# Performance work log

Hardware: AMD Instinct MI355X
Metric: run time of the kernel (lower is better)

The kernel has to match this reference:

```python
import jax, jax.numpy as jnp
import numpy as np

B, L, D = 16, 1024, 1024
OUT_LEN = 24
N_LAYERS = 3
CYCLE = L
LN_EPS = 1e-5


def _make_pe(seq_len, hidden, cycle):
    # pe[t, j] = 2*pi*t/cycle, then sin on even cols, cos on odd cols
    t = jnp.arange(seq_len, dtype=jnp.float32)[:, None]
    base = (2.0 * jnp.pi * t / cycle) * jnp.ones((1, hidden), jnp.float32)
    cols = jnp.arange(hidden)
    return jnp.where((cols % 2 == 0)[None, :], jnp.sin(base), jnp.cos(base))


def setup_inputs() -> dict:
    key = jax.random.key(0)
    ks = jax.random.split(key, 12)
    s = 0.02
    return {
        "x": jax.random.normal(ks[0], (B, L, D), jnp.float32),
        "pe": _make_pe(L, D, CYCLE),
        "w1": jax.random.normal(ks[1], (N_LAYERS, D, D), jnp.float32) * s,
        "b1": jnp.zeros((N_LAYERS, D), jnp.float32),
        "w2": jax.random.normal(ks[2], (N_LAYERS, D, D), jnp.float32) * s,
        "b2": jnp.zeros((N_LAYERS, D), jnp.float32),
        "ln_g": jnp.ones((N_LAYERS, D), jnp.float32),
        "ln_b": jnp.zeros((N_LAYERS, D), jnp.float32),
        "fc_w": jax.random.normal(ks[3], (1, D), jnp.float32) * s,
        "fc_b": jnp.zeros((1,), jnp.float32),
        "final_w": jax.random.normal(ks[4], (OUT_LEN, L), jnp.float32) * s,
        "final_b": jnp.zeros((OUT_LEN,), jnp.float32),
    }


def _layer_norm(y, g, b):
    mu = jnp.mean(y, axis=-1, keepdims=True)
    var = jnp.mean((y - mu) ** 2, axis=-1, keepdims=True)
    return (y - mu) * jax.lax.rsqrt(var + LN_EPS) * g + b


def reference(x, pe, w1, b1, w2, b2, ln_g, ln_b, fc_w, fc_b, final_w, final_b):
    d = x.shape[-1]
    scale = 1.0 / jnp.sqrt(jnp.float32(d))
    # positional add (pe[:, :seq_len]; here L == D so this is the full buffer)
    h = x + pe[:, : x.shape[1]]
    attns = []
    for l in range(w1.shape[0]):
        # hand-rolled bmm-softmax-bmm self-attention (q = k = v = h)
        scores = jnp.einsum("bqd,bkd->bqk", h, h) * scale  # (B, L, L)
        a = jax.nn.softmax(scores, axis=-1)
        ctx = jnp.einsum("bqk,bkd->bqd", a, h)
        # position-wise FFN with hidden == D, residual over ctx, then LN
        ff = jnp.maximum(ctx @ w1[l].T + b1[l], 0.0) @ w2[l].T + b2[l]
        h = _layer_norm(ctx + ff, ln_g[l], ln_b[l])
        attns.append(a)
    # final head: D -> 1, squeeze, then L -> OUT_LEN over the sequence dim
    z = (h @ fc_w.T + fc_b)[..., 0]  # (B, L)
    out = z @ final_w.T + final_b    # (B, OUT_LEN)
    return (out, jnp.stack(attns))
```

## Files before the change

### kernel.cpp

```cpp
#include <hip/hip_runtime.h>

typedef unsigned short u16;
typedef __attribute__((ext_vector_type(8))) short short8;
typedef __attribute__((ext_vector_type(4))) float f32x4;
typedef __attribute__((ext_vector_type(4))) unsigned short u16x4;

__device__ __forceinline__ float bf2f(u16 u){
  union { unsigned int i; float f; } x; x.i = ((unsigned int)u) << 16; return x.f;
}
__device__ __forceinline__ u16 f2bf(float f){
  union { float f; unsigned int i; } x; x.f = f;
  return (u16)((x.i + 0x7fffu + ((x.i >> 16) & 1u)) >> 16);
}
__device__ __forceinline__ void async16(const void* g, void* s){
  __builtin_amdgcn_global_load_lds((const __attribute__((address_space(1))) void*)g,
                                   (__attribute__((address_space(3))) void*)s, 16, 0, 0);
}

__global__ __launch_bounds__(256) void k_split(const float* __restrict__ s, u16* __restrict__ d){
  long i = ((long)blockIdx.x * 256 + threadIdx.x) * 4;
  f32x4 v = *(const f32x4*)(s + i);
  u16x4 hh;
  #pragma unroll
  for (int j=0;j<4;j++) hh[j] = f2bf(v[j]);
  *(u16x4*)(d+i) = hh;
}

__global__ __launch_bounds__(256) void k_addpe(const float* __restrict__ x, const float* __restrict__ pe,
                                               u16* __restrict__ d){
  long i = ((long)blockIdx.x * 256 + threadIdx.x) * 4;
  f32x4 xv = *(const f32x4*)(x + i);
  f32x4 pv = *(const f32x4*)(pe + (i & 1048575));
  u16x4 hh;
  #pragma unroll
  for (int j=0;j<4;j++) hh[j] = f2bf(xv[j]+pv[j]);
  *(u16x4*)(d+i) = hh;
}

__global__ __launch_bounds__(256) void k_transpose(const u16* __restrict__ in, u16* __restrict__ outp){
  __shared__ u16 tile[64][68];
  const long b = blockIdx.z;
  const int d0 = blockIdx.x * 64, l0 = blockIdx.y * 64;
  const long ibase = b * 1048576l;
  const int t = threadIdx.x;
  const int cr = t >> 4;
  const int cc = (t & 15) * 4;
  #pragma unroll
  for (int rr=0; rr<4; rr++){
    int row = cr + rr*16;
    u16x4 v = *(const u16x4*)(in + ibase + (long)(l0+row)*1024 + d0 + cc);
    *(u16x4*)&tile[row][cc] = v;
  }
  __syncthreads();
  #pragma unroll
  for (int rr=0; rr<4; rr++){
    int drow = cr + rr*16;
    u16x4 y;
    y[0] = tile[cc+0][drow];
    y[1] = tile[cc+1][drow];
    y[2] = tile[cc+2][drow];
    y[3] = tile[cc+3][drow];
    *(u16x4*)(outp + ibase + (long)(d0+drow)*1024 + l0 + cc) = y;
  }
}

template<int MODE>
__global__ __launch_bounds__(256) void gemm1(
    const u16* __restrict__ aB, const u16* __restrict__ bB,
    int K, int lda, int ldb, int ldc,
    long strideA, long strideB, long strideC,
    int gridN, int gridM,
    float scale, const float* __restrict__ bias,
    const u16* __restrict__ res,
    float* __restrict__ cF, u16* __restrict__ cB)
{
  __shared__ __align__(16) u16 sm[8192];
  const int t = threadIdx.x;
  const int w = t >> 6;
  const int lane = t & 63;

  const int p = blockIdx.x;
  const int chunk = gridDim.x >> 3;
  const int id = (p & 7) * chunk + (p >> 3);
  const int per = gridN * gridM;
  const long bz = id / per;
  const int rem = id % per;
  const int m0 = (rem / gridN) << 7, n0 = (rem % gridN) << 7;

  const u16* a = aB + bz * strideA;
  const u16* b = bB + bz * strideB;

  const int rA0 = t >> 2;
  const int rA1 = 64 + rA0;
  const int s0 = (t & 3) ^ ((rA0 >> 1) & 3);
  const int s1 = (t & 3) ^ ((rA1 >> 1) & 3);
  const u16* gA0 = a + (long)(m0 + rA0) * lda + s0 * 8;
  const u16* gA1 = a + (long)(m0 + rA1) * lda + s1 * 8;
  const u16* gB0 = b + (long)(n0 + rA0) * ldb + s0 * 8;
  const u16* gB1 = b + (long)(n0 + rA1) * ldb + s1 * 8;
  u16* ldsW = sm + (w << 9);

  f32x4 acc[4][4];
  #pragma unroll
  for (int i=0;i<4;i++)
    #pragma unroll
    for (int j=0;j<4;j++) acc[i][j] = (f32x4){0.f,0.f,0.f,0.f};

  const int fr = lane & 15, fs = lane >> 4;
  int offA[4], offB[4];
  #pragma unroll
  for (int i=0;i<4;i++){
    int ra = (w >> 1)*64 + i*16 + fr;
    offA[i] = ra*32 + (fs ^ ((ra>>1)&3))*8;
    int rb = (w & 1)*64 + i*16 + fr;
    offB[i] = rb*32 + (fs ^ ((rb>>1)&3))*8;
  }

  for (int k0 = 0; k0 < K; k0 += 32){
    async16(gA0 + k0, ldsW + 0);
    async16(gA1 + k0, ldsW + 2048);
    async16(gB0 + k0, ldsW + 4096);
    async16(gB1 + k0, ldsW + 6144);
    __syncthreads();
    short8 ah[4];
    #pragma unroll
    for (int i=0;i<4;i++) ah[i] = *(const short8*)(sm + offA[i]);
    #pragma unroll
    for (int j=0;j<4;j++){
      short8 bh = *(const short8*)(sm + 4096 + offB[j]);
      #pragma unroll
      for (int i=0;i<4;i++)
        acc[i][j] = __builtin_amdgcn_mfma_f32_16x16x32_bf16(ah[i], bh, acc[i][j], 0,0,0);
    }
    __syncthreads();
  }

  const long cBase = bz * strideC;
  const int colb = n0 + (w & 1)*64 + fr;
  const int rowb = m0 + (w >> 1)*64 + fs*4;
  #pragma unroll
  for (int j=0;j<4;j++){
    const int c = colb + j*16;
    float bv = 0.f;
    if constexpr (MODE == 2 || MODE == 3) bv = bias[c];
    #pragma unroll
    for (int i=0;i<4;i++){
      #pragma unroll
      for (int q=0;q<4;q++){
        const int r = rowb + i*16 + q;
        const long idx = cBase + (long)r*ldc + c;
        float v = acc[i][j][q];
        if constexpr (MODE == 0){
          cF[idx] = v * scale;
        } else if constexpr (MODE == 1){
          cB[idx] = f2bf(v);
        } else if constexpr (MODE == 2){
          cB[idx] = f2bf(fmaxf(v + bv, 0.f));
        } else {
          cF[idx] = v + bv + bf2f(res[idx]);
        }
      }
    }
  }
}

__global__ __launch_bounds__(256) void k_softmax(float* __restrict__ p, u16* __restrict__ pB){
  const long row = blockIdx.x;
  float* pr = p + row * 1024;
  const int t = threadIdx.x, w = t >> 6, lane = t & 63;
  __shared__ float rA[4], rB[4];
  f32x4 v = *(const f32x4*)(pr + t*4);
  float m = fmaxf(fmaxf(v[0],v[1]), fmaxf(v[2],v[3]));
  #pragma unroll
  for (int off=32; off; off>>=1) m = fmaxf(m, __shfl_xor(m, off));
  if (lane==0) rA[w] = m;
  __syncthreads();
  m = fmaxf(fmaxf(rA[0],rA[1]), fmaxf(rA[2],rA[3]));
  float e[4]; float s = 0.f;
  #pragma unroll
  for (int j=0;j<4;j++){ e[j] = expf(v[j]-m); s += e[j]; }
  #pragma unroll
  for (int off=32; off; off>>=1) s += __shfl_xor(s, off);
  if (lane==0) rB[w] = s;
  __syncthreads();
  s = rB[0]+rB[1]+rB[2]+rB[3];
  const float inv = 1.0f / s;
  f32x4 o; u16x4 hh;
  #pragma unroll
  for (int j=0;j<4;j++){
    float pv = e[j]*inv; o[j] = pv; hh[j] = f2bf(pv);
  }
  *(f32x4*)(pr + t*4) = o;
  *(u16x4*)(pB + row*1024 + t*4) = hh;
}

__global__ __launch_bounds__(256) void k_ln(const float* __restrict__ r,
                                            const float* __restrict__ g, const float* __restrict__ b,
                                            u16* __restrict__ h){
  const long row = blockIdx.x;
  const float* rr = r + row * 1024;
  const int t = threadIdx.x, w = t >> 6, lane = t & 63;
  __shared__ float rA[4], rB[4];
  f32x4 v = *(const f32x4*)(rr + t*4);
  float s = v[0]+v[1]+v[2]+v[3];
  #pragma unroll
  for (int off=32; off; off>>=1) s += __shfl_xor(s, off);
  if (lane==0) rA[w] = s;
  __syncthreads();
  const float mu = (rA[0]+rA[1]+rA[2]+rA[3]) * (1.0f/1024.0f);
  float sq = 0.f;
  #pragma unroll
  for (int j=0;j<4;j++){ float d = v[j]-mu; sq += d*d; }
  #pragma unroll
  for (int off=32; off; off>>=1) sq += __shfl_xor(sq, off);
  if (lane==0) rB[w] = sq;
  __syncthreads();
  const float var = (rB[0]+rB[1]+rB[2]+rB[3]) * (1.0f/1024.0f);
  const float inv = rsqrtf(var + 1e-5f);
  u16x4 hh;
  #pragma unroll
  for (int j=0;j<4;j++){
    int d = t*4+j;
    hh[j] = f2bf((v[j]-mu)*inv*g[d] + b[d]);
  }
  *(u16x4*)(h + row*1024 + t*4) = hh;
}

__global__ __launch_bounds__(256) void k_final1(const u16* __restrict__ h,
                                                const float* __restrict__ fw, const float* __restrict__ fb,
                                                float* __restrict__ z){
  const int row = blockIdx.x*4 + (threadIdx.x>>6);
  const int lane = threadIdx.x & 63;
  const long base = (long)row * 1024;
  const int d0 = lane * 16;
  float s = 0.f;
  #pragma unroll
  for (int j=0;j<16;j++){
    int d = d0 + j;
    s += bf2f(h[base+d]) * fw[d];
  }
  #pragma unroll
  for (int off=32; off; off>>=1) s += __shfl_xor(s, off);
  if (lane==0) z[row] = s + fb[0];
}

__global__ __launch_bounds__(256) void k_final2(const float* __restrict__ z,
                                                const float* __restrict__ fw, const float* __restrict__ fb,
                                                float* __restrict__ out){
  const int idx = blockIdx.x*4 + (threadIdx.x>>6);
  const int lane = threadIdx.x & 63;
  const int b = idx / 24, o = idx % 24;
  float s = 0.f;
  #pragma unroll
  for (int j=0;j<16;j++){
    int li = lane + j*64;
    s += z[b*1024 + li] * fw[o*1024 + li];
  }
  #pragma unroll
  for (int off=32; off; off>>=1) s += __shfl_xor(s, off);
  if (lane==0) out[idx] = s + fb[o];
}

extern "C" void kernel_launch(void* const* d_in, const int* in_sizes, int n_in,
                              void* d_out, int out_size, void* d_ws, size_t ws_size,
                              hipStream_t stream){
  const float* x   = (const float*)d_in[0];
  const float* pe  = (const float*)d_in[1];
  const float* w1  = (const float*)d_in[2];
  const float* b1  = (const float*)d_in[3];
  const float* w2  = (const float*)d_in[4];
  const float* b2  = (const float*)d_in[5];
  const float* lng = (const float*)d_in[6];
  const float* lnb = (const float*)d_in[7];
  const float* fcw = (const float*)d_in[8];
  const float* fcb = (const float*)d_in[9];
  const float* fw  = (const float*)d_in[10];
  const float* fb  = (const float*)d_in[11];
  float* out  = (float*)d_out;
  float* attn = out + 384;

  char* ws = (char*)d_ws;
  const long BB = 32l*1024*1024;
  u16* hB = (u16*)(ws + 0*BB);
  u16* tB = (u16*)(ws + 1*BB);
  u16* cB = (u16*)(ws + 2*BB);
  u16* pB = (u16*)(ws + 3*BB);
  float* rf = (float*)(ws + 4*BB);
  u16* w1B = (u16*)(ws + 6*BB);
  u16* w2B = w1B + 3l*1024*1024;
  float* z = (float*)(w2B + 3l*1024*1024);

  const long M1 = 1024l*1024;

  k_split<<<3072, 256, 0, stream>>>(w1, w1B);
  k_split<<<3072, 256, 0, stream>>>(w2, w2B);
  k_addpe<<<16384, 256, 0, stream>>>(x, pe, hB);
  k_transpose<<<dim3(16,16,16), 256, 0, stream>>>(hB, tB);

  for (int l = 0; l < 3; l++){
    float* sc = attn + (long)l*16*M1;
    gemm1<0><<<1024, 256, 0, stream>>>(hB, hB, 1024,1024,1024,1024,
        M1,M1,M1, 8,8, 0.03125f, nullptr, nullptr, sc, nullptr);
    k_softmax<<<16384, 256, 0, stream>>>(sc, pB);
    gemm1<1><<<1024, 256, 0, stream>>>(pB, tB, 1024,1024,1024,1024,
        M1,M1,M1, 8,8, 1.f, nullptr, nullptr, nullptr, cB);
    gemm1<2><<<1024, 256, 0, stream>>>(cB, w1B+l*M1, 1024,1024,1024,1024,
        0,0,0, 8,128, 1.f, b1+l*1024, nullptr, nullptr, pB);
    gemm1<3><<<1024, 256, 0, stream>>>(pB, w2B+l*M1, 1024,1024,1024,1024,
        0,0,0, 8,128, 1.f, b2+l*1024, cB, rf, nullptr);
    k_ln<<<16384, 256, 0, stream>>>(rf, lng+l*1024, lnb+l*1024, hB);
    if (l < 2) k_transpose<<<dim3(16,16,16), 256, 0, stream>>>(hB, tB);
  }

  k_final1<<<4096, 256, 0, stream>>>(hB, fcw, fcb, z);
  k_final2<<<96, 256, 0, stream>>>(z, fw, fb, out);
}
```

Baseline: 881.6 us.

## Replace 128x128 GEMM with 256x256 tile, 4-stage async LDS pipeline

Replaces the 256-thread 128x128-tile GEMM, which synchronized on every K step, with a 512-thread, 8-wave kernel computing 256x256 tiles. It keeps a 4-deep ring of LDS buffers filled by async global-to-LDS loads, uses explicit vmcnt waits and barriers, and raises wave priority around the MFMA bursts. The aim is to hide global load latency and raise data reuse per tile. In exchange it uses 128 KB of LDS and 128 accumulator floats per thread. It also hardcodes K=1024 (32 K-steps), so the grid drops to 256 blocks, which may underfill the 256 CUs.

```diff
diff --git a/kernel.cpp b/kernel.cpp
--- a/kernel.cpp
+++ b/kernel.cpp
@@ -65,89 +65,156 @@
 }
 
 template<int MODE>
-__global__ __launch_bounds__(256) void gemm1(
+__global__ __launch_bounds__(512, 2) void gemm8(
     const u16* __restrict__ aB, const u16* __restrict__ bB,
-    int K, int lda, int ldb, int ldc,
-    long strideA, long strideB, long strideC,
-    int gridN, int gridM,
+    int per, long sA, long sB, long sC,
+    int lda, int ldb, int ldc,
     float scale, const float* __restrict__ bias,
     const u16* __restrict__ res,
     float* __restrict__ cF, u16* __restrict__ cB)
 {
-  __shared__ __align__(16) u16 sm[8192];
+  __shared__ __align__(16) u16 sm[65536];
   const int t = threadIdx.x;
-  const int w = t >> 6;
-  const int lane = t & 63;
+  const int w = t >> 6, lane = t & 63;
+  const int wm = w >> 2, wn = w & 3;
+  const int fr = lane & 15, fs = lane >> 4;
 
   const int p = blockIdx.x;
   const int chunk = gridDim.x >> 3;
   const int id = (p & 7) * chunk + (p >> 3);
-  const int per = gridN * gridM;
   const long bz = id / per;
   const int rem = id % per;
-  const int m0 = (rem / gridN) << 7, n0 = (rem % gridN) << 7;
-
-  const u16* a = aB + bz * strideA;
-  const u16* b = bB + bz * strideB;
-
-  const int rA0 = t >> 2;
-  const int rA1 = 64 + rA0;
-  const int s0 = (t & 3) ^ ((rA0 >> 1) & 3);
-  const int s1 = (t & 3) ^ ((rA1 >> 1) & 3);
-  const u16* gA0 = a + (long)(m0 + rA0) * lda + s0 * 8;
-  const u16* gA1 = a + (long)(m0 + rA1) * lda + s1 * 8;
-  const u16* gB0 = b + (long)(n0 + rA0) * ldb + s0 * 8;
-  const u16* gB1 = b + (long)(n0 + rA1) * ldb + s1 * 8;
-  u16* ldsW = sm + (w << 9);
-
-  f32x4 acc[4][4];
-  #pragma unroll
-  for (int i=0;i<4;i++)
+  const int m0 = (rem >> 2) << 8, n0 = (rem & 3) << 8;
+
+  const u16* a = aB + bz * sA;
+  const u16* b = bB + bz * sB;
+
+  const int urow = t >> 2;
+  const int col8 = ((t & 3) ^ ((t >> 3) & 3)) * 8;
+  const u16* gA0 = a + (long)(m0 + urow) * lda + col8;
+  const u16* gA1 = a + (long)(m0 + 128 + urow) * lda + col8;
+  const u16* gB0 = b + (long)(n0 + urow) * ldb + col8;
+  const u16* gB1 = b + (long)(n0 + 128 + urow) * ldb + col8;
+  u16* dA0 = sm + (w << 9);
+  u16* dA1 = sm + 4096 + (w << 9);
+  u16* dB0 = sm + 8192 + (w << 9);
+  u16* dB1 = sm + 12288 + (w << 9);
+
+  int offA[8], offB[4];
+  #pragma unroll
+  for (int i=0;i<8;i++){
+    int row = wm*128 + i*16 + fr;
+    int sl = fs ^ ((row >> 1) & 3);
+    offA[i] = row*32 + sl*8;
+  }
+  #pragma unroll
+  for (int j=0;j<4;j++){
+    int row = wn*64 + j*16 + fr;
+    int sl = fs ^ ((row >> 1) & 3);
+    offB[j] = 8192 + row*32 + sl*8;
+  }
+
+  f32x4 acc[8][4];
+  #pragma unroll
+  for (int i=0;i<8;i++)
     #pragma unroll
     for (int j=0;j<4;j++) acc[i][j] = (f32x4){0.f,0.f,0.f,0.f};
 
-  const int fr = lane & 15, fs = lane >> 4;
-  int offA[4], offB[4];
-  #pragma unroll
-  for (int i=0;i<4;i++){
-    int ra = (w >> 1)*64 + i*16 + fr;
-    offA[i] = ra*32 + (fs ^ ((ra>>1)&3))*8;
-    int rb = (w & 1)*64 + i*16 + fr;
-    offB[i] = rb*32 + (fs ^ ((rb>>1)&3))*8;
-  }
-
-  for (int k0 = 0; k0 < K; k0 += 32){
-    async16(gA0 + k0, ldsW + 0);
-    async16(gA1 + k0, ldsW + 2048);
-    async16(gB0 + k0, ldsW + 4096);
-    async16(gB1 + k0, ldsW + 6144);
-    __syncthreads();
-    short8 ah[4];
-    #pragma unroll
-    for (int i=0;i<4;i++) ah[i] = *(const short8*)(sm + offA[i]);
-    #pragma unroll
-    for (int j=0;j<4;j++){
-      short8 bh = *(const short8*)(sm + 4096 + offB[j]);
-      #pragma unroll
-      for (int i=0;i<4;i++)
-        acc[i][j] = __builtin_amdgcn_mfma_f32_16x16x32_bf16(ah[i], bh, acc[i][j], 0,0,0);
-    }
-    __syncthreads();
-  }
-
-  const long cBase = bz * strideC;
-  const int colb = n0 + (w & 1)*64 + fr;
-  const int rowb = m0 + (w >> 1)*64 + fs*4;
+  #pragma unroll
+  for (int pb=0; pb<3; ++pb){
+    const int kb = pb*32, sb = pb*16384;
+    async16(gA0+kb, dA0+sb); async16(gA1+kb, dA1+sb);
+    async16(gB0+kb, dB0+sb); async16(gB1+kb, dB1+sb);
+  }
+  gA0 += 96; gA1 += 96; gB0 += 96; gB1 += 96;
+  asm volatile("s_waitcnt vmcnt(8)" ::: "memory");
+  __builtin_amdgcn_s_barrier();
+  __builtin_amdgcn_sched_barrier(0);
+
+#define KT_COMPUTE(SMB)                                                        \
+    short8 aF[8];                                                              \
+    _Pragma("unroll")                                                          \
+    for (int i=0;i<8;i++) aF[i] = *(const short8*)((SMB) + offA[i]);           \
+    short8 bF0 = *(const short8*)((SMB) + offB[0]);                            \
+    short8 bF1 = *(const short8*)((SMB) + offB[1]);
+
+#define KT_MFMA01                                                              \
+    __builtin_amdgcn_s_barrier();                                              \
+    __builtin_amdgcn_sched_barrier(0);                                         \
+    __builtin_amdgcn_s_setprio(1);                                             \
+    _Pragma("unroll")                                                          \
+    for (int i=0;i<8;i++){                                                     \
+      acc[i][0] = __builtin_amdgcn_mfma_f32_16x16x32_bf16(aF[i], bF0, acc[i][0], 0,0,0); \
+      acc[i][1] = __builtin_amdgcn_mfma_f32_16x16x32_bf16(aF[i], bF1, acc[i][1], 0,0,0); \
+    }                                                                          \
+    __builtin_amdgcn_s_setprio(0);                                             \
+    __builtin_amdgcn_s_barrier();
+
+#define KT_MFMA23(SMB)                                                         \
+    short8 bF2 = *(const short8*)((SMB) + offB[2]);                            \
+    short8 bF3 = *(const short8*)((SMB) + offB[3]);                            \
+    __builtin_amdgcn_s_setprio(1);                                             \
+    _Pragma("unroll")                                                          \
+    for (int i=0;i<8;i++){                                                     \
+      acc[i][2] = __builtin_amdgcn_mfma_f32_16x16x32_bf16(aF[i], bF2, acc[i][2], 0,0,0); \
+      acc[i][3] = __builtin_amdgcn_mfma_f32_16x16x32_bf16(aF[i], bF3, acc[i][3], 0,0,0); \
+    }                                                                          \
+    __builtin_amdgcn_s_setprio(0);
+
+  for (int kt = 0; kt < 29; ++kt){
+    const u16* smb = sm + (kt & 3)*16384;
+    const int sb = ((kt + 3) & 3)*16384;
+    KT_COMPUTE(smb)
+    async16(gA0, dA0+sb); async16(gA1, dA1+sb);
+    async16(gB0, dB0+sb); async16(gB1, dB1+sb);
+    gA0 += 32; gA1 += 32; gB0 += 32; gB1 += 32;
+    KT_MFMA01
+    KT_MFMA23(smb)
+    asm volatile("s_waitcnt vmcnt(8)" ::: "memory");
+    __builtin_amdgcn_s_barrier();
+    __builtin_amdgcn_sched_barrier(0);
+  }
+  {
+    const u16* smb = sm + (29 & 3)*16384;
+    KT_COMPUTE(smb)
+    KT_MFMA01
+    KT_MFMA23(smb)
+    asm volatile("s_waitcnt vmcnt(4)" ::: "memory");
+    __builtin_amdgcn_s_barrier();
+    __builtin_amdgcn_sched_barrier(0);
+  }
+  {
+    const u16* smb = sm + (30 & 3)*16384;
+    KT_COMPUTE(smb)
+    KT_MFMA01
+    KT_MFMA23(smb)
+    asm volatile("s_waitcnt vmcnt(0)" ::: "memory");
+    __builtin_amdgcn_s_barrier();
+    __builtin_amdgcn_sched_barrier(0);
+  }
+  {
+    const u16* smb = sm + (31 & 3)*16384;
+    KT_COMPUTE(smb)
+    KT_MFMA01
+    KT_MFMA23(smb)
+  }
+#undef KT_COMPUTE
+#undef KT_MFMA01
+#undef KT_MFMA23
+
+  const long cBase = bz * sC;
+  const int rb = m0 + wm*128 + fs*4;
+  const int cb = n0 + wn*64 + fr;
   #pragma unroll
   for (int j=0;j<4;j++){
-    const int c = colb + j*16;
+    const int c = cb + j*16;
     float bv = 0.f;
     if constexpr (MODE == 2 || MODE == 3) bv = bias[c];
     #pragma unroll
-    for (int i=0;i<4;i++){
+    for (int i=0;i<8;i++){
       #pragma unroll
       for (int q=0;q<4;q++){
-        const int r = rowb + i*16 + q;
+        const int r = rb + i*16 + q;
         const long idx = cBase + (long)r*ldc + c;
         float v = acc[i][j][q];
         if constexpr (MODE == 0){
@@ -299,15 +366,15 @@
 
   for (int l = 0; l < 3; l++){
     float* sc = attn + (long)l*16*M1;
-    gemm1<0><<<1024, 256, 0, stream>>>(hB, hB, 1024,1024,1024,1024,
-        M1,M1,M1, 8,8, 0.03125f, nullptr, nullptr, sc, nullptr);
+    gemm8<0><<<256, 512, 0, stream>>>(hB, hB, 16, M1,M1,M1, 1024,1024,1024,
+        0.03125f, nullptr, nullptr, sc, nullptr);
     k_softmax<<<16384, 256, 0, stream>>>(sc, pB);
-    gemm1<1><<<1024, 256, 0, stream>>>(pB, tB, 1024,1024,1024,1024,
-        M1,M1,M1, 8,8, 1.f, nullptr, nullptr, nullptr, cB);
-    gemm1<2><<<1024, 256, 0, stream>>>(cB, w1B+l*M1, 1024,1024,1024,1024,
-        0,0,0, 8,128, 1.f, b1+l*1024, nullptr, nullptr, pB);
-    gemm1<3><<<1024, 256, 0, stream>>>(pB, w2B+l*M1, 1024,1024,1024,1024,
-        0,0,0, 8,128, 1.f, b2+l*1024, cB, rf, nullptr);
+    gemm8<1><<<256, 512, 0, stream>>>(pB, tB, 16, M1,M1,M1, 1024,1024,1024,
+        1.f, nullptr, nullptr, nullptr, cB);
+    gemm8<2><<<256, 512, 0, stream>>>(cB, w1B+l*M1, 256, 0,0,0, 1024,1024,1024,
+        1.f, b1+l*1024, nullptr, nullptr, pB);
+    gemm8<3><<<256, 512, 0, stream>>>(pB, w2B+l*M1, 256, 0,0,0, 1024,1024,1024,
+        1.f, b2+l*1024, cB, rf, nullptr);
     k_ln<<<16384, 256, 0, stream>>>(rf, lng+l*1024, lnb+l*1024, hB);
     if (l < 2) k_transpose<<<dim3(16,16,16), 256, 0, stream>>>(hB, tB);
   }
```

New measurement: 745.0 us. -15.5%, faster.
